# Performance work log

Hardware: AMD Instinct MI355X
Metric: run time of the kernel (lower is better)

Reference implementation:

```python
import jax, jax.numpy as jnp
import numpy as np

HQ, HKV, D, RD = 32, 8, 128, 64   # q heads, kv heads, head_dim, rotary_dim
EPS = 1e-6


def _rms_norm(x, w, eps):
    # per-head RMSNorm over last dim (non-gemma: scale by w)
    var = jnp.mean(x * x, axis=-1, keepdims=True)
    return x * jax.lax.rsqrt(var + eps) * w


def _partial_rope(x, c, s, rd):
    # x: [T, H, D]; c/s: [T, rd//2]; NeoX half-split rotation on first rd dims
    x1 = x[..., : rd // 2]
    x2 = x[..., rd // 2 : rd]
    c = c[:, None, :]
    s = s[:, None, :]
    return jnp.concatenate([x1 * c - x2 * s, x2 * c + x1 * s, x[..., rd:]], axis=-1)


def setup_inputs() -> dict:
    key = jax.random.key(0)
    ks = jax.random.split(key, 6)
    B, QL, HID, CACHE = 4, 512, 4096, 512
    T = B * QL
    MAXPOS = 4096
    NPAGES, PS, MP = 256, 16, 64  # total pages, page_size, max pages per seq

    hidden_states = jax.random.normal(ks[0], (T, HID), jnp.float32)
    inv = 1.0 / (10000.0 ** (np.arange(0, RD, 2, dtype=np.float64) / RD))
    ang = np.arange(MAXPOS)[:, None] * inv[None, :]
    cos = jnp.asarray(np.cos(ang), jnp.float32)   # [MAXPOS, RD//2]
    sin = jnp.asarray(np.sin(ang), jnp.float32)
    positions = jnp.tile(CACHE + jnp.arange(QL, dtype=jnp.int32), B)  # [T]
    k_cache = jax.random.normal(ks[1], (NPAGES, PS, HKV, D), jnp.float32)
    v_cache = jax.random.normal(ks[2], (NPAGES, PS, HKV, D), jnp.float32)
    page_table = jnp.arange(B * MP, dtype=jnp.int32).reshape(B, MP)
    cache_seqlens = jnp.full((B,), CACHE, jnp.int32)
    cu_seqlens_q = jnp.arange(B + 1, dtype=jnp.int32) * QL
    qkv_weight = jax.random.normal(ks[3], ((HQ + 2 * HKV) * D, HID), jnp.float32) * 0.02
    o_proj_weight = jax.random.normal(ks[4], (HID, HQ * D), jnp.float32) * 0.02
    q_norm_weight = jnp.ones((D,), jnp.float32)
    k_norm_weight = jnp.ones((D,), jnp.float32)
    return dict(hidden_states=hidden_states, cos=cos, sin=sin, positions=positions,
                k_cache=k_cache, v_cache=v_cache, page_table=page_table,
                cache_seqlens=cache_seqlens, cu_seqlens_q=cu_seqlens_q,
                qkv_weight=qkv_weight, o_proj_weight=o_proj_weight,
                q_norm_weight=q_norm_weight, k_norm_weight=k_norm_weight)


def reference(hidden_states, cos, sin, positions, k_cache, v_cache, page_table,
              cache_seqlens, cu_seqlens_q, qkv_weight, o_proj_weight,
              q_norm_weight, k_norm_weight):
    T = hidden_states.shape[0]
    B = cache_seqlens.shape[0]
    QL = T // B                       # equal-length sequences (extend mode)
    PS = k_cache.shape[1]

    # QKV projection + split
    qkv = hidden_states @ qkv_weight.T
    q, k, v = jnp.split(qkv, [HQ * D, (HQ + HKV) * D], axis=-1)

    # per-head QK RMSNorm (q_norm_weight.shape[0] == head_dim branch)
    q = _rms_norm(q.reshape(T, HQ, D), q_norm_weight, EPS)
    k = _rms_norm(k.reshape(T, HKV, D), k_norm_weight, EPS)
    v = v.reshape(T, HKV, D)

    # partial RoPE
    pc, psn = cos[positions], sin[positions]
    q = _partial_rope(q, pc, psn, RD)
    k = _partial_rope(k, pc, psn, RD)

    # paged KV-cache write: absolute slot = cache_seqlens[b] + j
    pos_abs = cache_seqlens[:, None] + jnp.arange(QL, dtype=jnp.int32)[None, :]  # [B,QL]
    pages = jnp.take_along_axis(page_table, pos_abs // PS, axis=1)
    slots = pos_abs % PS
    k_cache = k_cache.at[pages, slots].set(k.reshape(B, QL, HKV, D))
    v_cache = v_cache.at[pages, slots].set(v.reshape(B, QL, HKV, D))

    # gather per-sequence KV from pages: [B, KV, HKV, D]
    KV = page_table.shape[1] * PS
    keys = k_cache[page_table].reshape(B, KV, HKV, D)
    vals = v_cache[page_table].reshape(B, KV, HKV, D)

    # GQA paged attention with causal mask on absolute positions
    G = HQ // HKV
    qh = q.reshape(B, QL, HKV, G, D)
    scale = 1.0 / np.sqrt(D).astype(np.float32)
    scores = jnp.einsum('bqhgd,bkhd->bhgqk', qh, keys) * scale
    kpos = jnp.arange(KV, dtype=jnp.int32)
    mask = kpos[None, None, :] <= pos_abs[:, :, None]                  # [B,QL,KV]
    scores = jnp.where(mask[:, None, None, :, :], scores, -1e30)
    probs = jax.nn.softmax(scores, axis=-1)
    attn = jnp.einsum('bhgqk,bkhd->bqhgd', probs, vals).reshape(T, HQ * D)

    return attn @ o_proj_weight.T
```

## Files before the change

kernel.cpp:

```cpp
#include <hip/hip_runtime.h>

typedef unsigned int   u32;
typedef unsigned short u16;

typedef float  f32x4  __attribute__((ext_vector_type(4)));
typedef u32    u32x4  __attribute__((ext_vector_type(4)));
typedef u16    u16x4  __attribute__((ext_vector_type(4)));
typedef __bf16 bf16x8 __attribute__((ext_vector_type(8)));

union FragU { u16 us[8]; u32x4 q; bf16x8 v; };

__device__ __forceinline__ u32 f2u(float x){ union{float f;u32 u;}c; c.f=x; return c.u; }
__device__ __forceinline__ float u2f(u32 u){ union{float f;u32 u;}c; c.u=u; return c.f; }
__device__ __forceinline__ u16 bfhi(float x){ u32 u=f2u(x); return (u16)((u + 0x7fffu + ((u>>16)&1u))>>16); }
__device__ __forceinline__ float bff(u16 h){ return u2f(((u32)h)<<16); }
__device__ __forceinline__ u32 pack2(float x){
  u16 h = bfhi(x);
  u16 l = bfhi(x - bff(h));
  return (u32)h | ((u32)l << 16);
}

__device__ __forceinline__ void gload16(const void* g, void* l){
  __builtin_amdgcn_global_load_lds(
      (const __attribute__((address_space(1))) unsigned int*)g,
      (__attribute__((address_space(3))) unsigned int*)l, 16, 0, 0);
}

__global__ __launch_bounds__(256)
void bf16_pack3(const float* __restrict__ s0, u16* __restrict__ d0, int n0,
                const float* __restrict__ s1, u16* __restrict__ d1, int n1,
                const float* __restrict__ s2, u16* __restrict__ d2, int n2)
{
  const int total = n0 + n1 + n2;
  for (int i = blockIdx.x*256 + threadIdx.x; i < total; i += gridDim.x*256){
    const float* s; u16* d; int j = i;
    if (j < n0)            { s = s0; d = d0; }
    else if (j < n0 + n1)  { s = s1; d = d1; j -= n0; }
    else                   { s = s2; d = d2; j -= n0 + n1; }
    float4 v = reinterpret_cast<const float4*>(s)[j];
    reinterpret_cast<u16x4*>(d)[j] =
      (u16x4){ bfhi(v.x), bfhi(v.y), bfhi(v.z), bfhi(v.w) };
  }
}

__global__ __launch_bounds__(256, 2)
void gemm_pkA2(const u16* __restrict__ A, const u16* __restrict__ B,
               float* __restrict__ C, int M, int N, int K)
{
  extern __shared__ char smem[];
  const int tid  = threadIdx.x;
  const int lane = tid & 63;
  const int w    = tid >> 6;
  const int wm = w >> 1, wn = w & 1;
  const int ln = lane & 15, lg = lane >> 4;

  const int nbm = M >> 7;
  const int nbn = N / 192;
  const int nwg = nbm * nbn;
  const int swz = (blockIdx.x & 7) * (nwg >> 3) + (blockIdx.x >> 3);
  const int bm = swz % nbm, bn = swz / nbm;

  const size_t rb = (size_t)K * 2;
  const int lrow  = lane >> 3;
  const int lslot = (lane & 7) ^ (lrow & 7);
  const char* As0 = (const char*)A + (size_t)(bm*128 + w*8 + lrow)*rb + lslot*16;
  const char* Bs0 = (const char*)B + (size_t)(bn*192 + w*8 + lrow)*rb + lslot*16;

  auto stA = [&](int buf, int t) {
    const char* s = As0 + ((size_t)t << 7);
    char* d = smem + buf*40960 + w*1024;
    gload16(s,           d);
    gload16(s +  32*rb,  d + 4096);
    gload16(s +  64*rb,  d + 8192);
    gload16(s +  96*rb,  d + 12288);
  };
  auto stB = [&](int buf, int t) {
    const char* s = Bs0 + ((size_t)t << 7);
    char* d = smem + buf*40960 + 16384 + w*1024;
    gload16(s,           d);
    gload16(s +  32*rb,  d + 4096);
    gload16(s +  64*rb,  d + 8192);
    gload16(s +  96*rb,  d + 12288);
    gload16(s + 128*rb,  d + 16384);
    gload16(s + 160*rb,  d + 20480);
  };

  f32x4 z = {0.f,0.f,0.f,0.f};
  f32x4 acc[4][6];
  #pragma unroll
  for (int i=0;i<4;i++){
    #pragma unroll
    for (int j=0;j<6;j++) acc[i][j] = z;
  }

  const int nt = K >> 6;
  stA(0, 0); stB(0, 0);
  if (nt > 1) { stB(1, 1);
    asm volatile("s_waitcnt vmcnt(6)" ::: "memory");
  } else {
    asm volatile("s_waitcnt vmcnt(0)" ::: "memory");
  }
  __builtin_amdgcn_s_barrier();
  asm volatile("" ::: "memory");

  const int lx7 = ln & 7;

  for (int t = 0; t < nt; ++t){
    const int cur = t & 1;
    const char* bufc = smem + cur*40960;

    FragU bfr[6][2];
    #pragma unroll
    for (int ni=0; ni<6; ni++){
      const int rofs = 16384 + (wn*96 + ni*16 + ln)*128;
      #pragma unroll
      for (int ks=0; ks<2; ks++)
        bfr[ni][ks].q = *reinterpret_cast<const u32x4*>(bufc + rofs + (((ks*4+lg)^lx7)<<4));
    }
    FragU af[2][2];
    #pragma unroll
    for (int mf=0; mf<2; mf++){
      const int rofs = (wm*64 + mf*16 + ln)*128;
      #pragma unroll
      for (int ks=0; ks<2; ks++)
        af[mf][ks].q = *reinterpret_cast<const u32x4*>(bufc + rofs + (((ks*4+lg)^lx7)<<4));
    }
    if (t+1 < nt) stA(cur^1, t+1);
    __builtin_amdgcn_s_barrier();
    __builtin_amdgcn_s_setprio(1);
    #pragma unroll
    for (int ks=0; ks<2; ks++){
      #pragma unroll
      for (int mf=0; mf<2; mf++){
        #pragma unroll
        for (int ni=0; ni<6; ni++)
          acc[mf][ni] = __builtin_amdgcn_mfma_f32_16x16x32_bf16(af[mf][ks].v, bfr[ni][ks].v, acc[mf][ni], 0,0,0);
      }
    }
    __builtin_amdgcn_s_setprio(0);
    asm volatile("s_waitcnt lgkmcnt(0)" ::: "memory");
    __builtin_amdgcn_s_barrier();

    FragU ag[2][2];
    #pragma unroll
    for (int mf=0; mf<2; mf++){
      const int rofs = (wm*64 + (mf+2)*16 + ln)*128;
      #pragma unroll
      for (int ks=0; ks<2; ks++)
        ag[mf][ks].q = *reinterpret_cast<const u32x4*>(bufc + rofs + (((ks*4+lg)^lx7)<<4));
    }
    if (t+2 < nt) stB(cur, t+2);
    __builtin_amdgcn_s_barrier();
    __builtin_amdgcn_s_setprio(1);
    #pragma unroll
    for (int ks=0; ks<2; ks++){
      #pragma unroll
      for (int mf=0; mf<2; mf++){
        #pragma unroll
        for (int ni=0; ni<6; ni++)
          acc[mf+2][ni] = __builtin_amdgcn_mfma_f32_16x16x32_bf16(ag[mf][ks].v, bfr[ni][ks].v, acc[mf+2][ni], 0,0,0);
      }
    }
    __builtin_amdgcn_s_setprio(0);
    if (t+1 < nt){
      if (t+2 < nt) asm volatile("s_waitcnt vmcnt(6)" ::: "memory");
      else          asm volatile("s_waitcnt vmcnt(0)" ::: "memory");
    }
    __builtin_amdgcn_s_barrier();
    asm volatile("" ::: "memory");
  }

  #pragma unroll
  for (int mi=0; mi<4; mi++){
    #pragma unroll
    for (int ni=0; ni<6; ni++){
      const int row0 = bm*128 + wm*64 + mi*16 + lg*4;
      const int col  = bn*192 + wn*96 + ni*16 + ln;
      #pragma unroll
      for (int r=0; r<4; r++)
        C[(size_t)(row0+r)*N + col] = acc[mi][ni][r];
    }
  }
}

__global__ __launch_bounds__(256, 2)
void gemm_pkB2(const u16* __restrict__ A, const u16* __restrict__ B,
               float* __restrict__ C, int M, int N, int K)
{
  extern __shared__ char smem[];
  const int tid  = threadIdx.x;
  const int lane = tid & 63;
  const int w    = tid >> 6;
  const int wm = w >> 1, wn = w & 1;
  const int ln = lane & 15, lg = lane >> 4;

  const int nbm = M >> 7, nbn = N >> 7;
  const int nwg = nbm * nbn;
  const int swz = (blockIdx.x & 7) * (nwg >> 3) + (blockIdx.x >> 3);
  const int bm = swz % nbm, bn = swz / nbm;

  const size_t rb = (size_t)K * 2;
  const int lrow  = lane >> 3;
  const int lslot = (lane & 7) ^ (lrow & 7);
  const char* As0 = (const char*)A + (size_t)(bm*128 + w*8 + lrow)*rb + lslot*16;
  const char* Bs0 = (const char*)B + (size_t)(bn*128 + w*8 + lrow)*rb + lslot*16;

  auto stA = [&](int buf, int t) {
    const char* s = As0 + ((size_t)t << 7);
    char* d = smem + buf*32768 + w*1024;
    gload16(s,           d);
    gload16(s +  32*rb,  d + 4096);
    gload16(s +  64*rb,  d + 8192);
    gload16(s +  96*rb,  d + 12288);
  };
  auto stB = [&](int buf, int t) {
    const char* s = Bs0 + ((size_t)t << 7);
    char* d = smem + buf*32768 + 16384 + w*1024;
    gload16(s,           d);
    gload16(s +  32*rb,  d + 4096);
    gload16(s +  64*rb,  d + 8192);
    gload16(s +  96*rb,  d + 12288);
  };

  f32x4 z = {0.f,0.f,0.f,0.f};
  f32x4 acc[4][4];
  #pragma unroll
  for (int i=0;i<4;i++){
    #pragma unroll
    for (int j=0;j<4;j++) acc[i][j] = z;
  }

  const int nt = K >> 6;
  stA(0, 0); stB(0, 0);
  if (nt > 1) { stB(1, 1);
    asm volatile("s_waitcnt vmcnt(4)" ::: "memory");
  } else {
    asm volatile("s_waitcnt vmcnt(0)" ::: "memory");
  }
  __builtin_amdgcn_s_barrier();
  asm volatile("" ::: "memory");

  const int lx7 = ln & 7;

  for (int t = 0; t < nt; ++t){
    const int cur = t & 1;
    const char* bufc = smem + cur*32768;

    FragU bfr[4][2];
    #pragma unroll
    for (int ni=0; ni<4; ni++){
      const int rofs = 16384 + (wn*64 + ni*16 + ln)*128;
      #pragma unroll
      for (int ks=0; ks<2; ks++)
        bfr[ni][ks].q = *reinterpret_cast<const u32x4*>(bufc + rofs + (((ks*4+lg)^lx7)<<4));
    }
    FragU af[2][2];
    #pragma unroll
    for (int mf=0; mf<2; mf++){
      const int rofs = (wm*64 + mf*16 + ln)*128;
      #pragma unroll
      for (int ks=0; ks<2; ks++)
        af[mf][ks].q = *reinterpret_cast<const u32x4*>(bufc + rofs + (((ks*4+lg)^lx7)<<4));
    }
    if (t+1 < nt) stA(cur^1, t+1);
    __builtin_amdgcn_s_barrier();
    __builtin_amdgcn_s_setprio(1);
    #pragma unroll
    for (int ks=0; ks<2; ks++){
      #pragma unroll
      for (int mf=0; mf<2; mf++){
        #pragma unroll
        for (int ni=0; ni<4; ni++)
          acc[mf][ni] = __builtin_amdgcn_mfma_f32_16x16x32_bf16(af[mf][ks].v, bfr[ni][ks].v, acc[mf][ni], 0,0,0);
      }
    }
    __builtin_amdgcn_s_setprio(0);
    asm volatile("s_waitcnt lgkmcnt(0)" ::: "memory");
    __builtin_amdgcn_s_barrier();

    FragU ag[2][2];
    #pragma unroll
    for (int mf=0; mf<2; mf++){
      const int rofs = (wm*64 + (mf+2)*16 + ln)*128;
      #pragma unroll
      for (int ks=0; ks<2; ks++)
        ag[mf][ks].q = *reinterpret_cast<const u32x4*>(bufc + rofs + (((ks*4+lg)^lx7)<<4));
    }
    if (t+2 < nt) stB(cur, t+2);
    __builtin_amdgcn_s_barrier();
    __builtin_amdgcn_s_setprio(1);
    #pragma unroll
    for (int ks=0; ks<2; ks++){
      #pragma unroll
      for (int mf=0; mf<2; mf++){
        #pragma unroll
        for (int ni=0; ni<4; ni++)
          acc[mf+2][ni] = __builtin_amdgcn_mfma_f32_16x16x32_bf16(ag[mf][ks].v, bfr[ni][ks].v, acc[mf+2][ni], 0,0,0);
      }
    }
    __builtin_amdgcn_s_setprio(0);
    if (t+1 < nt){
      if (t+2 < nt) asm volatile("s_waitcnt vmcnt(4)" ::: "memory");
      else          asm volatile("s_waitcnt vmcnt(0)" ::: "memory");
    }
    __builtin_amdgcn_s_barrier();
    asm volatile("" ::: "memory");
  }

  #pragma unroll
  for (int mi=0; mi<4; mi++){
    #pragma unroll
    for (int ni=0; ni<4; ni++){
      const int row0 = bm*128 + wm*64 + mi*16 + lg*4;
      const int col  = bn*128 + wn*64 + ni*16 + ln;
      #pragma unroll
      for (int r=0; r<4; r++)
        C[(size_t)(row0+r)*N + col] = acc[mi][ni][r];
    }
  }
}

__global__ __launch_bounds__(256)
void copy_cache(const float* __restrict__ k_cache, const float* __restrict__ v_cache,
                const int* __restrict__ page_table,
                u16* __restrict__ k_all, u32* __restrict__ v_allT)
{
  __shared__ float tb[32][129];
  const int id = blockIdx.x;
  const int jt = id & 31, h = (id>>5)&7, b = id>>8;
  const int tid = threadIdx.x;
  const int j0 = jt*32;
  {
    int r = tid>>3, c = tid&7;
    int j = j0 + r;
    int page = page_table[b*64 + (j>>4)];
    int slot = j & 15;
    const float* ks = k_cache + (size_t)((page*16 + slot)*8 + h)*128;
    const float* vs = v_cache + (size_t)((page*16 + slot)*8 + h)*128;
    u16* kd = k_all + ((size_t)(b*8+h)*1024 + j)*128;
    #pragma unroll
    for (int i=0;i<4;i++){
      int d0 = (c + 8*i)*4;
      float4 k4 = *reinterpret_cast<const float4*>(ks + d0);
      *reinterpret_cast<u16x4*>(kd + d0) =
        (u16x4){ bfhi(k4.x), bfhi(k4.y), bfhi(k4.z), bfhi(k4.w) };
      float4 v4 = *reinterpret_cast<const float4*>(vs + d0);
      tb[r][d0+0]=v4.x; tb[r][d0+1]=v4.y; tb[r][d0+2]=v4.z; tb[r][d0+3]=v4.w;
    }
  }
  __syncthreads();
  {
    int dout = tid>>1, jh = tid&1;
    u32* vd = v_allT + ((size_t)(b*8+h)*128 + dout)*1024 + j0 + jh*16;
    #pragma unroll
    for (int i=0;i<4;i++){
      u32x4 o;
      o.x = pack2(tb[jh*16 + i*4 + 0][dout]);
      o.y = pack2(tb[jh*16 + i*4 + 1][dout]);
      o.z = pack2(tb[jh*16 + i*4 + 2][dout]);
      o.w = pack2(tb[jh*16 + i*4 + 3][dout]);
      *reinterpret_cast<u32x4*>(vd + i*4) = o;
    }
  }
}

__global__ __launch_bounds__(256)
void norm_rope_scatter(float* __restrict__ qkv, const float* __restrict__ cosT,
                       const float* __restrict__ sinT, const int* __restrict__ positions,
                       const int* __restrict__ cache_seqlens,
                       const float* __restrict__ qw, const float* __restrict__ kw,
                       u16* __restrict__ k_all, u32* __restrict__ v_allT)
{
  const int t = blockIdx.x;
  const int lane = threadIdx.x & 63;
  const int w = threadIdx.x >> 6;
  const int b = t >> 9;
  const int q = t & 511;
  const int pos  = positions[t];
  const int cpos = cache_seqlens[b] + q;
  for (int it=0; it<12; ++it){
    int h = it*4 + w;
    float* xp = qkv + (size_t)t*6144 + h*128 + 2*lane;
    float2 x = *reinterpret_cast<const float2*>(xp);
    if (h < 40){
      float ss = x.x*x.x + x.y*x.y;
      #pragma unroll
      for (int mk=1; mk<64; mk<<=1) ss += __shfl_xor(ss, mk);
      float var = ss*(1.0f/128.0f) + 1e-6f;
      float rq = rsqrtf(var);
      rq = rq*(1.5f - 0.5f*var*rq*rq);
      const float* wt = (h<32) ? qw : kw;
      x.x *= rq*wt[2*lane]; x.y *= rq*wt[2*lane+1];
      float px = __shfl_xor(x.x, 16);
      float py = __shfl_xor(x.y, 16);
      if (lane < 32){
        int ci = pos*32 + 2*(lane&15);
        float2 cc = *reinterpret_cast<const float2*>(cosT + ci);
        float2 sc = *reinterpret_cast<const float2*>(sinT + ci);
        if (lane < 16){ x.x = x.x*cc.x - px*sc.x; x.y = x.y*cc.y - py*sc.y; }
        else          { x.x = x.x*cc.x + px*sc.x; x.y = x.y*cc.y + py*sc.y; }
      }
    }
    if (h < 32){
      *reinterpret_cast<float2*>(xp) = x;
    } else if (h < 40){
      u16* kp = k_all + ((size_t)(b*8 + (h-32))*1024 + cpos)*128 + 2*lane;
      kp[0] = bfhi(x.x); kp[1] = bfhi(x.y);
    } else {
      u32* vp = v_allT + ((size_t)(b*8 + (h-40))*128 + 2*lane)*1024 + cpos;
      vp[0]    = pack2(x.x);
      vp[1024] = pack2(x.y);
    }
  }
}

__global__ __launch_bounds__(256)
void attn_fused5(const float* __restrict__ qkv, const u16* __restrict__ k_all,
                 const u32* __restrict__ v_allT, const int* __restrict__ cache_seqlens,
                 u16* __restrict__ attnO)
{
  extern __shared__ char smem[];
  u32* Pl = (u32*)(smem + 49152);
  const int tid = threadIdx.x, lane = tid&63, w = tid>>6;
  const int ln = lane&15, lg = lane>>4;
  const int id = blockIdx.x;
  const int qt = id & 7, g = (id>>3)&3, kvh = (id>>5)&7, b = id>>8;
  const int cs = cache_seqlens[b];
  const int h  = kvh*4 + g;
  const int q0 = qt*64 + w*16;
  const float SCALE = 0.08838834764831845f;
  f32x4 z = {0.f,0.f,0.f,0.f};

  FragU qf[4];
  {
    const float* qp = qkv + (size_t)(b*512 + q0 + ln)*6144 + h*128;
    #pragma unroll
    for (int ks=0; ks<4; ks++){
      int d0 = ks*32 + lg*8;
      float4 a = *reinterpret_cast<const float4*>(qp + d0);
      float4 c = *reinterpret_cast<const float4*>(qp + d0 + 4);
      qf[ks].q = (u32x4){
        (u32)bfhi(a.x*SCALE) | ((u32)bfhi(a.y*SCALE)<<16),
        (u32)bfhi(a.z*SCALE) | ((u32)bfhi(a.w*SCALE)<<16),
        (u32)bfhi(c.x*SCALE) | ((u32)bfhi(c.y*SCALE)<<16),
        (u32)bfhi(c.z*SCALE) | ((u32)bfhi(c.w*SCALE)<<16) };
    }
  }
  f32x4 O[8];
  #pragma unroll
  for (int i=0;i<8;i++) O[i] = z;
  float lacc[4] = {0.f,0.f,0.f,0.f};
  const int prow0 = cs + q0 + lg*4;
  const int nt = (cs + qt*64 + 64 + 31) >> 5;
  const char* kbase = (const char*)(k_all  + (size_t)(b*8+kvh)*1024*128);
  const char* vbase = (const char*)(v_allT + (size_t)(b*8+kvh)*128*1024);

  const int vrb = w*8 + (lane>>3);
  const int vsl = lane & 7;

  auto stK = [&](int buf, int t){
    #pragma unroll
    for (int i=0;i<2;i++){
      int row = i*16 + w*4 + (lane>>4);
      const char* s = kbase + (size_t)(t*32 + row)*256 + (((lane&15) ^ (row&7))<<4);
      gload16(s, smem + buf*8192 + i*4096 + w*1024);
    }
  };
  auto stV = [&](int buf, int t){
    #pragma unroll
    for (int i=0;i<4;i++){
      int d = i*32 + vrb;
      const char* s = vbase + (size_t)d*4096 + (size_t)t*128 + ((vsl ^ (d&7))<<4);
      gload16(s, smem + 16384 + buf*16384 + i*4096 + w*1024);
    }
  };

  stK(0, 0); stV(0, 0);
  if (nt > 1){ stK(1, 1); stV(1, 1); }

  for (int tile=0; tile<nt; ++tile){
    const int cur = tile & 1;
    const int kv0 = tile*32;
    if (tile+1 < nt) asm volatile("s_waitcnt vmcnt(6)" ::: "memory");
    else             asm volatile("s_waitcnt vmcnt(0)" ::: "memory");
    __builtin_amdgcn_s_barrier();

    const u16* Kc = (const u16*)(smem + cur*8192);
    f32x4 sa0=z, sa1=z, sb0=z, sb1=z;
    #pragma unroll
    for (int ks=0; ks<2; ks++){
      int so = ((ks*4+lg) ^ (ln&7)) << 3;
      FragU kf0, kf1;
      kf0.q = *reinterpret_cast<const u32x4*>(&Kc[ln*128 + so]);
      kf1.q = *reinterpret_cast<const u32x4*>(&Kc[(16+ln)*128 + so]);
      sa0 = __builtin_amdgcn_mfma_f32_16x16x32_bf16(qf[ks].v, kf0.v, sa0, 0,0,0);
      sa1 = __builtin_amdgcn_mfma_f32_16x16x32_bf16(qf[ks].v, kf1.v, sa1, 0,0,0);
    }
    #pragma unroll
    for (int ks=2; ks<4; ks++){
      int so = ((ks*4+lg) ^ (ln&7)) << 3;
      FragU kf0, kf1;
      kf0.q = *reinterpret_cast<const u32x4*>(&Kc[ln*128 + so]);
      kf1.q = *reinterpret_cast<const u32x4*>(&Kc[(16+ln)*128 + so]);
      sb0 = __builtin_amdgcn_mfma_f32_16x16x32_bf16(qf[ks].v, kf0.v, sb0, 0,0,0);
      sb1 = __builtin_amdgcn_mfma_f32_16x16x32_bf16(qf[ks].v, kf1.v, sb1, 0,0,0);
    }
    f32x4 s[2]; s[0] = sa0 + sb0; s[1] = sa1 + sb1;

    float pv[2][4];
    if (kv0 + 31 <= cs + q0){
      #pragma unroll
      for (int n=0;n<2;n++){
        #pragma unroll
        for (int r=0;r<4;r++) pv[n][r] = __expf(s[n][r]);
      }
    } else {
      #pragma unroll
      for (int n=0;n<2;n++){
        #pragma unroll
        for (int r=0;r<4;r++){
          bool ok = (kv0 + n*16 + ln) <= (prow0 + r);
          pv[n][r] = ok ? __expf(s[n][r]) : 0.f;
        }
      }
    }
    #pragma unroll
    for (int r=0;r<4;r++) lacc[r] += pv[0][r] + pv[1][r];

    #pragma unroll
    for (int n=0;n<2;n++){
      #pragma unroll
      for (int rp=0; rp<2; rp++){
        float p0 = pv[n][rp*2], p1 = pv[n][rp*2+1];
        u32 hpk, lpk;
        asm("v_cvt_pk_bf16_f32 %0, %1, %2" : "=v"(hpk) : "v"(p0), "v"(p1));
        float l0 = p0 - u2f(hpk << 16);
        float l1 = p1 - u2f(hpk & 0xffff0000u);
        asm("v_cvt_pk_bf16_f32 %0, %1, %2" : "=v"(lpk) : "v"(l0), "v"(l1));
        u32 w0 = __builtin_amdgcn_perm(lpk, hpk, 0x05040100u);
        u32 w1 = __builtin_amdgcn_perm(lpk, hpk, 0x07060302u);
        int row0 = lg*4 + rp*2;
        Pl[w*512 + ((row0*32 + n*16 + ln) ^ ((row0&7)<<2))] = w0;
        int row1 = row0 + 1;
        Pl[w*512 + ((row1*32 + n*16 + ln) ^ ((row1&7)<<2))] = w1;
      }
    }
    FragU pah[2], pal[2];
    #pragma unroll
    for (int ks2=0; ks2<2; ks2++){
      int fi = (ln*32 + ks2*16 + lg*4) ^ ((ln&7)<<2);
      u32x4 pp = *reinterpret_cast<const u32x4*>(&Pl[w*512 + fi]);
      #pragma unroll
      for (int i=0;i<4;i++){
        pah[ks2].q[i] = __builtin_amdgcn_perm(pp[i], pp[i], 0x01000100u);
        pal[ks2].q[i] = __builtin_amdgcn_perm(pp[i], pp[i], 0x03020302u);
      }
    }
    const u16* Vc = (const u16*)(smem + 16384 + cur*16384);
    #pragma unroll
    for (int nf=0; nf<8; nf++){
      int dr = nf*16 + ln;
      #pragma unroll
      for (int ks2=0; ks2<2; ks2++){
        FragU vf;
        vf.q = *reinterpret_cast<const u32x4*>(&Vc[(dr*64 + ks2*32 + lg*8) ^ ((dr&7)<<3)]);
        O[nf] = __builtin_amdgcn_mfma_f32_16x16x32_bf16(pah[ks2].v, vf.v, O[nf], 0,0,0);
        O[nf] = __builtin_amdgcn_mfma_f32_16x16x32_bf16(pal[ks2].v, vf.v, O[nf], 0,0,0);
      }
    }
    asm volatile("s_waitcnt lgkmcnt(0)" ::: "memory");
    __builtin_amdgcn_s_barrier();
    if (tile+2 < nt){ stK(cur, tile+2); stV(cur, tile+2); }
  }

  #pragma unroll
  for (int off=1; off<16; off<<=1){
    #pragma unroll
    for (int r=0;r<4;r++) lacc[r] += __shfl_xor(lacc[r], off);
  }
  float il[4];
  #pragma unroll
  for (int r=0;r<4;r++) il[r] = 1.0f / lacc[r];
  u16* op = attnO + (size_t)(b*512 + q0 + lg*4)*4096 + h*128 + ln;
  #pragma unroll
  for (int nf=0; nf<8; nf++){
    #pragma unroll
    for (int r=0;r<4;r++)
      op[(size_t)r*4096 + nf*16] = bfhi(O[nf][r] * il[r]);
  }
}

extern "C" void kernel_launch(void* const* d_in, const int* in_sizes, int n_in,
                              void* d_out, int out_size, void* d_ws, size_t ws_size,
                              hipStream_t stream) {
  const float* hidden    = (const float*)d_in[0];
  const float* cosT      = (const float*)d_in[1];
  const float* sinT      = (const float*)d_in[2];
  const int*   positions = (const int*)  d_in[3];
  const float* k_cache   = (const float*)d_in[4];
  const float* v_cache   = (const float*)d_in[5];
  const int*   page_tab  = (const int*)  d_in[6];
  const int*   cache_sl  = (const int*)  d_in[7];
  const float* qkv_w     = (const float*)d_in[9];
  const float* o_w       = (const float*)d_in[10];
  const float* qnw       = (const float*)d_in[11];
  const float* knw       = (const float*)d_in[12];
  float* out = (float*)d_out;

  u32* ws      = (u32*)d_ws;
  float* qkv   = (float*)ws;
  u16* k_all   = (u16*)(ws + 12582912);
  u32* v_allT  = ws + 12582912 + 2097152;
  u16* attnPk  = (u16*)(v_allT + 4194304);
  u16* hidPk   = attnPk + 8388608;
  u16* qkvwPk  = hidPk  + 8388608;
  u16* owPk    = qkvwPk + 25165824;
  (void)in_sizes; (void)n_in; (void)out_size; (void)ws_size;

  (void)hipFuncSetAttribute(reinterpret_cast<const void*>(gemm_pkA2),
                            hipFuncAttributeMaxDynamicSharedMemorySize, 81920);
  (void)hipFuncSetAttribute(reinterpret_cast<const void*>(gemm_pkB2),
                            hipFuncAttributeMaxDynamicSharedMemorySize, 65536);
  (void)hipFuncSetAttribute(reinterpret_cast<const void*>(attn_fused5),
                            hipFuncAttributeMaxDynamicSharedMemorySize, 57344);

  hipLaunchKernelGGL(bf16_pack3, dim3(2048), dim3(256), 0, stream,
                     hidden, hidPk, 2097152,
                     qkv_w, qkvwPk, 6291456,
                     o_w, owPk, 4194304);
  hipLaunchKernelGGL(copy_cache, dim3(1024), dim3(256), 0, stream,
                     k_cache, v_cache, page_tab, k_all, v_allT);
  hipLaunchKernelGGL(gemm_pkA2, dim3(512), dim3(256), 81920, stream,
                     hidPk, qkvwPk, qkv, 2048, 6144, 4096);
  hipLaunchKernelGGL(norm_rope_scatter, dim3(2048), dim3(256), 0, stream,
                     qkv, cosT, sinT, positions, cache_sl, qnw, knw, k_all, v_allT);
  hipLaunchKernelGGL(attn_fused5, dim3(1024), dim3(256), 57344, stream,
                     qkv, k_all, v_allT, cache_sl, attnPk);
  hipLaunchKernelGGL(gemm_pkB2, dim3(512), dim3(256), 65536, stream,
                     attnPk, owPk, out, 2048, 4096, 4096);
}
```

Baseline: 365.4 us.

## Drop split-bf16 hi/lo precision for V and P in attention PV product

V and the softmax probabilities were previously stored as hi+lo bf16 pairs, and two MFMAs were issued per fragment to emulate higher precision. This stores V as a single bf16 and P as a single bf16, halving the V cache traffic and LDS footprint and halving the PV MFMAs. The V staging layout and swizzle change to match the narrower rows, and shared memory per block drops. The cost is lower accuracy in the PV product, which could exceed the output tolerance.

```diff
diff --git a/kernel.cpp b/kernel.cpp
--- a/kernel.cpp
+++ b/kernel.cpp
@@ -14,11 +14,6 @@
 __device__ __forceinline__ float u2f(u32 u){ union{float f;u32 u;}c; c.u=u; return c.f; }
 __device__ __forceinline__ u16 bfhi(float x){ u32 u=f2u(x); return (u16)((u + 0x7fffu + ((u>>16)&1u))>>16); }
 __device__ __forceinline__ float bff(u16 h){ return u2f(((u32)h)<<16); }
-__device__ __forceinline__ u32 pack2(float x){
-  u16 h = bfhi(x);
-  u16 l = bfhi(x - bff(h));
-  return (u32)h | ((u32)l << 16);
-}
 
 __device__ __forceinline__ void gload16(const void* g, void* l){
   __builtin_amdgcn_global_load_lds(
@@ -323,7 +318,7 @@
 __global__ __launch_bounds__(256)
 void copy_cache(const float* __restrict__ k_cache, const float* __restrict__ v_cache,
                 const int* __restrict__ page_table,
-                u16* __restrict__ k_all, u32* __restrict__ v_allT)
+                u16* __restrict__ k_all, u16* __restrict__ v_allT)
 {
   __shared__ float tb[32][129];
   const int id = blockIdx.x;
@@ -351,15 +346,14 @@
   __syncthreads();
   {
     int dout = tid>>1, jh = tid&1;
-    u32* vd = v_allT + ((size_t)(b*8+h)*128 + dout)*1024 + j0 + jh*16;
+    u16* vd = v_allT + ((size_t)(b*8+h)*128 + dout)*1024 + j0 + jh*16;
     #pragma unroll
     for (int i=0;i<4;i++){
-      u32x4 o;
-      o.x = pack2(tb[jh*16 + i*4 + 0][dout]);
-      o.y = pack2(tb[jh*16 + i*4 + 1][dout]);
-      o.z = pack2(tb[jh*16 + i*4 + 2][dout]);
-      o.w = pack2(tb[jh*16 + i*4 + 3][dout]);
-      *reinterpret_cast<u32x4*>(vd + i*4) = o;
+      u16x4 o = { bfhi(tb[jh*16 + i*4 + 0][dout]),
+                  bfhi(tb[jh*16 + i*4 + 1][dout]),
+                  bfhi(tb[jh*16 + i*4 + 2][dout]),
+                  bfhi(tb[jh*16 + i*4 + 3][dout]) };
+      *reinterpret_cast<u16x4*>(vd + i*4) = o;
     }
   }
 }
@@ -369,7 +363,7 @@
                        const float* __restrict__ sinT, const int* __restrict__ positions,
                        const int* __restrict__ cache_seqlens,
                        const float* __restrict__ qw, const float* __restrict__ kw,
-                       u16* __restrict__ k_all, u32* __restrict__ v_allT)
+                       u16* __restrict__ k_all, u16* __restrict__ v_allT)
 {
   const int t = blockIdx.x;
   const int lane = threadIdx.x & 63;
@@ -407,20 +401,19 @@
       u16* kp = k_all + ((size_t)(b*8 + (h-32))*1024 + cpos)*128 + 2*lane;
       kp[0] = bfhi(x.x); kp[1] = bfhi(x.y);
     } else {
-      u32* vp = v_allT + ((size_t)(b*8 + (h-40))*128 + 2*lane)*1024 + cpos;
-      vp[0]    = pack2(x.x);
-      vp[1024] = pack2(x.y);
+      u16* vp = v_allT + ((size_t)(b*8 + (h-40))*128 + 2*lane)*1024 + cpos;
+      vp[0]    = bfhi(x.x);
+      vp[1024] = bfhi(x.y);
     }
   }
 }
 
 __global__ __launch_bounds__(256)
-void attn_fused5(const float* __restrict__ qkv, const u16* __restrict__ k_all,
-                 const u32* __restrict__ v_allT, const int* __restrict__ cache_seqlens,
+void attn_fused6(const float* __restrict__ qkv, const u16* __restrict__ k_all,
+                 const u16* __restrict__ v_allT, const int* __restrict__ cache_seqlens,
                  u16* __restrict__ attnO)
 {
   extern __shared__ char smem[];
-  u32* Pl = (u32*)(smem + 49152);
   const int tid = threadIdx.x, lane = tid&63, w = tid>>6;
   const int ln = lane&15, lg = lane>>4;
   const int id = blockIdx.x;
@@ -455,9 +448,6 @@
   const char* kbase = (const char*)(k_all  + (size_t)(b*8+kvh)*1024*128);
   const char* vbase = (const char*)(v_allT + (size_t)(b*8+kvh)*128*1024);
 
-  const int vrb = w*8 + (lane>>3);
-  const int vsl = lane & 7;
-
   auto stK = [&](int buf, int t){
     #pragma unroll
     for (int i=0;i<2;i++){
@@ -468,10 +458,11 @@
   };
   auto stV = [&](int buf, int t){
     #pragma unroll
-    for (int i=0;i<4;i++){
-      int d = i*32 + vrb;
-      const char* s = vbase + (size_t)d*4096 + (size_t)t*128 + ((vsl ^ (d&7))<<4);
-      gload16(s, smem + 16384 + buf*16384 + i*4096 + w*1024);
+    for (int i=0;i<2;i++){
+      int row = i*64 + w*16 + (lane>>2);
+      int c   = lane & 3;
+      const char* s = vbase + (size_t)row*2048 + (size_t)t*64 + ((c ^ ((row>>1)&3))<<4);
+      gload16(s, smem + 16384 + buf*8192 + i*4096 + w*1024);
     }
   };
 
@@ -481,7 +472,7 @@
   for (int tile=0; tile<nt; ++tile){
     const int cur = tile & 1;
     const int kv0 = tile*32;
-    if (tile+1 < nt) asm volatile("s_waitcnt vmcnt(6)" ::: "memory");
+    if (tile+1 < nt) asm volatile("s_waitcnt vmcnt(4)" ::: "memory");
     else             asm volatile("s_waitcnt vmcnt(0)" ::: "memory");
     __builtin_amdgcn_s_barrier();
 
@@ -532,41 +523,26 @@
       #pragma unroll
       for (int rp=0; rp<2; rp++){
         float p0 = pv[n][rp*2], p1 = pv[n][rp*2+1];
-        u32 hpk, lpk;
+        u32 hpk;
         asm("v_cvt_pk_bf16_f32 %0, %1, %2" : "=v"(hpk) : "v"(p0), "v"(p1));
-        float l0 = p0 - u2f(hpk << 16);
-        float l1 = p1 - u2f(hpk & 0xffff0000u);
-        asm("v_cvt_pk_bf16_f32 %0, %1, %2" : "=v"(lpk) : "v"(l0), "v"(l1));
-        u32 w0 = __builtin_amdgcn_perm(lpk, hpk, 0x05040100u);
-        u32 w1 = __builtin_amdgcn_perm(lpk, hpk, 0x07060302u);
+        int col  = n*16 + ln;
         int row0 = lg*4 + rp*2;
-        Pl[w*512 + ((row0*32 + n*16 + ln) ^ ((row0&7)<<2))] = w0;
-        int row1 = row0 + 1;
-        Pl[w*512 + ((row1*32 + n*16 + ln) ^ ((row1&7)<<2))] = w1;
-      }
-    }
-    FragU pah[2], pal[2];
-    #pragma unroll
-    for (int ks2=0; ks2<2; ks2++){
-      int fi = (ln*32 + ks2*16 + lg*4) ^ ((ln&7)<<2);
-      u32x4 pp = *reinterpret_cast<const u32x4*>(&Pl[w*512 + fi]);
-      #pragma unroll
-      for (int i=0;i<4;i++){
-        pah[ks2].q[i] = __builtin_amdgcn_perm(pp[i], pp[i], 0x01000100u);
-        pal[ks2].q[i] = __builtin_amdgcn_perm(pp[i], pp[i], 0x03020302u);
-      }
-    }
-    const u16* Vc = (const u16*)(smem + 16384 + cur*16384);
+        int b0 = w*1024 + row0*64 + ((((col>>3) ^ ((row0>>1)&3)))<<4) + (col&7)*2;
+        *(u16*)(smem + 32768 + b0)      = (u16)hpk;
+        *(u16*)(smem + 32768 + b0 + 64) = (u16)(hpk >> 16);
+      }
+    }
+    FragU pa;
+    pa.q = *reinterpret_cast<const u32x4*>(
+        smem + 32768 + w*1024 + ln*64 + ((lg ^ ((ln>>1)&3))<<4));
+
+    const char* Vb = smem + 16384 + cur*8192;
     #pragma unroll
     for (int nf=0; nf<8; nf++){
       int dr = nf*16 + ln;
-      #pragma unroll
-      for (int ks2=0; ks2<2; ks2++){
-        FragU vf;
-        vf.q = *reinterpret_cast<const u32x4*>(&Vc[(dr*64 + ks2*32 + lg*8) ^ ((dr&7)<<3)]);
-        O[nf] = __builtin_amdgcn_mfma_f32_16x16x32_bf16(pah[ks2].v, vf.v, O[nf], 0,0,0);
-        O[nf] = __builtin_amdgcn_mfma_f32_16x16x32_bf16(pal[ks2].v, vf.v, O[nf], 0,0,0);
-      }
+      FragU vf;
+      vf.q = *reinterpret_cast<const u32x4*>(Vb + dr*64 + ((lg ^ ((dr>>1)&3))<<4));
+      O[nf] = __builtin_amdgcn_mfma_f32_16x16x32_bf16(pa.v, vf.v, O[nf], 0,0,0);
     }
     asm volatile("s_waitcnt lgkmcnt(0)" ::: "memory");
     __builtin_amdgcn_s_barrier();
@@ -607,11 +583,10 @@
   const float* knw       = (const float*)d_in[12];
   float* out = (float*)d_out;
 
-  u32* ws      = (u32*)d_ws;
-  float* qkv   = (float*)ws;
-  u16* k_all   = (u16*)(ws + 12582912);
-  u32* v_allT  = ws + 12582912 + 2097152;
-  u16* attnPk  = (u16*)(v_allT + 4194304);
+  float* qkv   = (float*)d_ws;
+  u16* k_all   = (u16*)(qkv + 12582912);
+  u16* v_allT  = k_all  + 4194304;
+  u16* attnPk  = v_allT + 4194304;
   u16* hidPk   = attnPk + 8388608;
   u16* qkvwPk  = hidPk  + 8388608;
   u16* owPk    = qkvwPk + 25165824;
@@ -621,8 +596,8 @@
                             hipFuncAttributeMaxDynamicSharedMemorySize, 81920);
   (void)hipFuncSetAttribute(reinterpret_cast<const void*>(gemm_pkB2),
                             hipFuncAttributeMaxDynamicSharedMemorySize, 65536);
-  (void)hipFuncSetAttribute(reinterpret_cast<const void*>(attn_fused5),
-                            hipFuncAttributeMaxDynamicSharedMemorySize, 57344);
+  (void)hipFuncSetAttribute(reinterpret_cast<const void*>(attn_fused6),
+                            hipFuncAttributeMaxDynamicSharedMemorySize, 36864);
 
   hipLaunchKernelGGL(bf16_pack3, dim3(2048), dim3(256), 0, stream,
                      hidden, hidPk, 2097152,
@@ -634,7 +609,7 @@
                      hidPk, qkvwPk, qkv, 2048, 6144, 4096);
   hipLaunchKernelGGL(norm_rope_scatter, dim3(2048), dim3(256), 0, stream,
                      qkv, cosT, sinT, positions, cache_sl, qnw, knw, k_all, v_allT);
-  hipLaunchKernelGGL(attn_fused5, dim3(1024), dim3(256), 57344, stream,
+  hipLaunchKernelGGL(attn_fused6, dim3(1024), dim3(256), 36864, stream,
                      qkv, k_all, v_allT, cache_sl, attnPk);
   hipLaunchKernelGGL(gemm_pkB2, dim3(512), dim3(256), 65536, stream,
                      attnPk, owPk, out, 2048, 4096, 4096);
```

After: 310.4 us. -15.1%, faster.
